# Kernel tuning notes

Measured on AMD Instinct MI355X. Metric: run time of the kernel, lower is better.

Reference implementation:

```python
import jax, jax.numpy as jnp
import numpy as np

N = 1_000_000          # number of query points
POINT_DIMS = 2         # (x, y) coordinates
NUM_EMB = 6572         # number of video frames
EMB_DIM = 32
HIDDEN = 128


def setup_inputs() -> dict:
    key = jax.random.key(0)
    ks = jax.random.split(key, 10)
    x = jax.random.uniform(ks[0], (N, POINT_DIMS), dtype=jnp.float32)
    # fractional frame index in [0, NUM_EMB - 1)
    embeddings = jax.random.uniform(ks[1], (N,), dtype=jnp.float32) * (NUM_EMB - 1)
    em_table = jax.random.normal(ks[2], (NUM_EMB, EMB_DIM), dtype=jnp.float32) * 0.1
    in0 = POINT_DIMS + EMB_DIM
    W0 = jax.random.normal(ks[3], (in0, HIDDEN), dtype=jnp.float32) / np.sqrt(in0)
    b0 = jax.random.normal(ks[4], (HIDDEN,), dtype=jnp.float32) * 0.01
    W1 = jax.random.normal(ks[5], (HIDDEN, HIDDEN), dtype=jnp.float32) / np.sqrt(HIDDEN)
    b1 = jax.random.normal(ks[6], (HIDDEN,), dtype=jnp.float32) * 0.01
    W2 = jax.random.normal(ks[7], (HIDDEN, 1), dtype=jnp.float32) / np.sqrt(HIDDEN)
    b2 = jax.random.normal(ks[8], (1,), dtype=jnp.float32) * 0.01
    return {"x": x, "embeddings": embeddings, "em_table": em_table,
            "W0": W0, "b0": b0, "W1": W1, "b1": b1, "W2": W2, "b2": b2}


def reference(x, embeddings, em_table, W0, b0, W1, b1, W2, b2):
    num_emb = em_table.shape[0]
    em1 = embeddings.astype(jnp.int32)                       # floor (inputs >= 0)
    em2 = jnp.minimum(em1 + 1, num_emb - 1)                  # clamp(em1+1, max=E-1)
    res = (embeddings - em1.astype(jnp.float32))[:, None]    # [N, 1]
    e1 = em_table[em1]                                       # [N, 32] gather
    e2 = em_table[em2]                                       # [N, 32] gather
    em = e1 + (e2 - e1) * res                                # lerp
    h = jnp.concatenate((x, em), axis=1) @ W0 + b0           # [N, 128]
    h = jnp.clip(h, 0.0, 1.0)
    h = jnp.clip(h @ W1 + b1, 0.0, 1.0)
    out = jax.nn.sigmoid(h @ W2 + b2)                        # [N, 1]
    return out
```

## Files before the change

### kernel.cpp

```cpp
#include <hip/hip_runtime.h>
#include <hip/hip_bf16.h>


using bf16x8 = __attribute__((ext_vector_type(8))) short;
using f32x4  = __attribute__((ext_vector_type(4))) float;

#define NPTS    1000000
#define NUMEMB  6572
#define HID     128
#define M_IT    64
#define A0S     72
#define H0S     136
#define TILES   (NPTS / M_IT)
#define NBLOCKS 1024

__device__ __forceinline__ unsigned short bf16r(float f) {
    unsigned u;
    __builtin_memcpy(&u, &f, 4);
    u = (u + 0x7fffu + ((u >> 16) & 1u)) >> 16;
    return (unsigned short)u;
}
__device__ __forceinline__ unsigned pk2(float a, float b) {
    float2 f2; f2.x = a; f2.y = b;
    __hip_bfloat162 h = __float22bfloat162_rn(f2);
    unsigned u;
    __builtin_memcpy(&u, &h, 4);
    return u;
}
__device__ __forceinline__ unsigned pk2c(float a, float b) {
    unsigned r;
    asm("v_cvt_pk_bf16_f32 %0, %1, %2 clamp" : "=v"(r) : "v"(a), "v"(b));
    return r;
}

__global__ __launch_bounds__(256, 4)
void mlp_fused(const float* __restrict__ x,
               const float* __restrict__ emb,
               const float* __restrict__ em_table,
               const float* __restrict__ W0, const float* __restrict__ b0,
               const float* __restrict__ W1, const float* __restrict__ b1,
               const float* __restrict__ W2, const float* __restrict__ b2,
               float* __restrict__ out)
{
    __shared__ __align__(16) unsigned short A0[M_IT * A0S];
    __shared__ __align__(16) unsigned short H0[M_IT * H0S];

    const int tid  = threadIdx.x;
    const int lane = tid & 63;
    const int nq   = tid >> 6;
    const int q    = lane >> 4;
    const int cl   = lane & 15;
    const int p    = tid >> 2;
    const int s    = tid & 3;

    for (int i = tid; i < M_IT * A0S; i += 256) A0[i] = 0;

    const int hcol = nq * 32 + (cl >> 2) * 8 + (cl & 3);
    bf16x8 w0t[2][2];
    for (int hb = 0; hb < 2; ++hb)
        for (int kt = 0; kt < 2; ++kt) {
            const int col = hcol + hb * 4;
            bf16x8 v;
            #pragma unroll
            for (int e = 0; e < 8; ++e) {
                const int k = kt * 32 + q * 8 + e;
                float val = 0.f;
                if (k < 32)       val = W0[(2 + k) * HID + col];
                else if (k == 32) val = W0[0 * HID + col];
                else if (k == 33) val = W0[1 * HID + col];
                v[e] = (short)bf16r(val);
            }
            w0t[hb][kt] = v;
        }

    bf16x8 w1r[2][4];
    for (int hb = 0; hb < 2; ++hb)
        for (int kk = 0; kk < 4; ++kk) {
            const int kt  = (nq + kk) & 3;
            const int col = hcol + hb * 4;
            bf16x8 v;
            #pragma unroll
            for (int e = 0; e < 8; ++e) {
                const int k = kt * 32 + q * 8 + e;
                v[e] = (short)bf16r(W1[k * HID + col]);
            }
            w1r[hb][kk] = v;
        }

    f32x4 b0q[2], b1q[2];
    for (int hb = 0; hb < 2; ++hb)
        for (int r = 0; r < 4; ++r) {
            const int h = nq * 32 + q * 8 + hb * 4 + r;
            b0q[hb][r] = b0[h];
            b1q[hb][r] = b1[h];
        }
    bf16x8 w2f;
    #pragma unroll
    for (int e = 0; e < 8; ++e)
        w2f[e] = (cl == 0) ? (short)bf16r(W2[nq * 32 + q * 8 + e]) : (short)0;
    const float bias2 = b2[0];

    int t = blockIdx.x;
    float  feA;
    float2 xvA = {0.f, 0.f};
    {
        const int gp = t * M_IT + p;
        feA = emb[gp];
        if (s == 0) xvA = *(const float2*)(x + 2 * gp);
    }

    __syncthreads();

    for (; t < TILES; t += gridDim.x) {
        const int base = t * M_IT;

        {
            const int e1 = (int)feA;
            const int e2 = (e1 + 1 < NUMEMB) ? e1 + 1 : NUMEMB - 1;
            const float r = feA - (float)e1;
            const float4* p1 = (const float4*)(em_table + e1 * 32 + s * 8);
            const float4* p2 = (const float4*)(em_table + e2 * 32 + s * 8);
            const float4 a0v = p1[0], a1v = p1[1];
            const float4 c0v = p2[0], c1v = p2[1];
            uint4 d;
            d.x = pk2(a0v.x + (c0v.x - a0v.x) * r, a0v.y + (c0v.y - a0v.y) * r);
            d.y = pk2(a0v.z + (c0v.z - a0v.z) * r, a0v.w + (c0v.w - a0v.w) * r);
            d.z = pk2(a1v.x + (c1v.x - a1v.x) * r, a1v.y + (c1v.y - a1v.y) * r);
            d.w = pk2(a1v.z + (c1v.z - a1v.z) * r, a1v.w + (c1v.w - a1v.w) * r);
            *(uint4*)&A0[p * A0S + s * 8] = d;
            if (s == 0) *(unsigned*)&A0[p * A0S + 32] = pk2(xvA.x, xvA.y);
        }
        __syncthreads();

        f32x4 acc[4][2];
        #pragma unroll
        for (int pb = 0; pb < 4; ++pb) {
            const bf16x8 bf0 = *(const bf16x8*)&A0[(pb * 16 + cl) * A0S + q * 8];
            const bf16x8 bf1 = *(const bf16x8*)&A0[(pb * 16 + cl) * A0S + 32 + q * 8];
            #pragma unroll
            for (int hb = 0; hb < 2; ++hb) {
                f32x4 a = __builtin_amdgcn_mfma_f32_16x16x32_bf16(
                    w0t[hb][0], bf0, b0q[hb], 0, 0, 0);
                acc[pb][hb] = __builtin_amdgcn_mfma_f32_16x16x32_bf16(
                    w0t[hb][1], bf1, a, 0, 0, 0);
            }
        }

        {
            int t1 = t + gridDim.x; if (t1 >= TILES) t1 = t;
            const int gp = t1 * M_IT + p;
            feA = emb[gp];
            if (s == 0) xvA = *(const float2*)(x + 2 * gp);
        }

        #pragma unroll
        for (int pb = 0; pb < 4; ++pb) {
            const f32x4 v0 = acc[pb][0], v1 = acc[pb][1];
            uint4 w;
            w.x = pk2c(v0[0], v0[1]);
            w.y = pk2c(v0[2], v0[3]);
            w.z = pk2c(v1[0], v1[1]);
            w.w = pk2c(v1[2], v1[3]);
            *(uint4*)&H0[(pb * 16 + cl) * H0S + nq * 32 + q * 8] = w;
        }
        __syncthreads();

        #pragma unroll
        for (int kk = 0; kk < 4; ++kk) {
            const int kcol = (((nq + kk) & 3) << 5) + q * 8;
            #pragma unroll
            for (int pb = 0; pb < 4; ++pb) {
                bf16x8 bfrag = *(const bf16x8*)
                    &H0[(pb * 16 + cl) * H0S + kcol];
                #pragma unroll
                for (int hb = 0; hb < 2; ++hb)
                    acc[pb][hb] = __builtin_amdgcn_mfma_f32_16x16x32_bf16(
                        w1r[hb][kk], bfrag,
                        kk == 0 ? b1q[hb] : acc[pb][hb], 0, 0, 0);
            }
        }

        const f32x4 zero = {0.f, 0.f, 0.f, 0.f};
        #pragma unroll
        for (int pb = 0; pb < 4; ++pb) {
            const f32x4 v0 = acc[pb][0], v1 = acc[pb][1];
            uint4 w;
            w.x = pk2c(v0[0], v0[1]);
            w.y = pk2c(v0[2], v0[3]);
            w.z = pk2c(v1[0], v1[1]);
            w.w = pk2c(v1[2], v1[3]);
            bf16x8 hf;
            __builtin_memcpy(&hf, &w, 16);
            const f32x4 z4 = __builtin_amdgcn_mfma_f32_16x16x32_bf16(
                w2f, hf, zero, 0, 0, 0);
            if (q == 0)
                *(float*)((char*)A0 + (pb * 16 + cl) * 144 + 128 + nq * 4) = z4[0];
        }
        __syncthreads();

        if (tid < 64) {
            const float4 pv = *(const float4*)((const char*)A0 + tid * 144 + 128);
            const float zz = bias2 + pv.x + pv.y + pv.z + pv.w;
            out[base + tid] = __builtin_amdgcn_rcpf(1.f + __expf(-zz));
        }
    }
}

extern "C" void kernel_launch(void* const* d_in, const int* in_sizes, int n_in,
                              void* d_out, int out_size, void* d_ws, size_t ws_size,
                              hipStream_t stream) {
    const float* x   = (const float*)d_in[0];
    const float* emb = (const float*)d_in[1];
    const float* emt = (const float*)d_in[2];
    const float* W0  = (const float*)d_in[3];
    const float* b0  = (const float*)d_in[4];
    const float* W1  = (const float*)d_in[5];
    const float* b1  = (const float*)d_in[6];
    const float* W2  = (const float*)d_in[7];
    const float* b2  = (const float*)d_in[8];
    mlp_fused<<<NBLOCKS, 256, 0, stream>>>(x, emb, emt, W0, b0, W1, b1, W2, b2,
                                           (float*)d_out);
}
```

Before: 136.0 us.

## Restructure MLP into single-wave blocks with register-resident hidden layers and gather prefetch

Each block becomes one 64-lane wave that handles 16 points per step and holds all W0/W1 fragments in registers. The first-layer activations pass directly as MFMA B-operands for layer two, so the LDS H0 staging and all block-wide barriers go away. The embedding gather is software-pipelined two chunks ahead and uses a double-buffered A0 tile. In exchange, register pressure rises sharply (w1t alone is 32 bf16x8 vectors), which may limit occupancy or cause spills. Only 1024 single-wave blocks are launched, so latency hiding depends on the prefetch.

```diff
diff --git a/kernel.cpp b/kernel.cpp
--- a/kernel.cpp
+++ b/kernel.cpp
@@ -8,11 +8,11 @@
 #define NPTS    1000000
 #define NUMEMB  6572
 #define HID     128
-#define M_IT    64
 #define A0S     72
-#define H0S     136
-#define TILES   (NPTS / M_IT)
+#define CHUNKS  62500
+#define LASTC   (CHUNKS - 1)
 #define NBLOCKS 1024
+#define STRIDE  1024
 
 __device__ __forceinline__ unsigned short bf16r(float f) {
     unsigned u;
@@ -33,7 +33,7 @@
     return r;
 }
 
-__global__ __launch_bounds__(256, 4)
+__global__ __launch_bounds__(64, 1)
 void mlp_fused(const float* __restrict__ x,
                const float* __restrict__ emb,
                const float* __restrict__ em_table,
@@ -42,24 +42,22 @@
                const float* __restrict__ W2, const float* __restrict__ b2,
                float* __restrict__ out)
 {
-    __shared__ __align__(16) unsigned short A0[M_IT * A0S];
-    __shared__ __align__(16) unsigned short H0[M_IT * H0S];
-
-    const int tid  = threadIdx.x;
-    const int lane = tid & 63;
-    const int nq   = tid >> 6;
-    const int q    = lane >> 4;
-    const int cl   = lane & 15;
-    const int p    = tid >> 2;
-    const int s    = tid & 3;
-
-    for (int i = tid; i < M_IT * A0S; i += 256) A0[i] = 0;
-
-    const int hcol = nq * 32 + (cl >> 2) * 8 + (cl & 3);
-    bf16x8 w0t[2][2];
-    for (int hb = 0; hb < 2; ++hb)
+    __shared__ __align__(16) unsigned short A0[2 * 16 * A0S];
+
+    const int lane = threadIdx.x;
+    const int q  = lane >> 4;
+    const int cl = lane & 15;
+    const int p  = lane >> 2;
+    const int s  = lane & 3;
+
+    for (int i = lane; i < 2 * 16 * A0S; i += 64) A0[i] = 0;
+
+    bf16x8 w0t[8][2];
+    #pragma unroll
+    for (int ob = 0; ob < 8; ++ob) {
+        const int col = (ob >> 1) * 32 + (cl >> 2) * 8 + (ob & 1) * 4 + (cl & 3);
+        #pragma unroll
         for (int kt = 0; kt < 2; ++kt) {
-            const int col = hcol + hb * 4;
             bf16x8 v;
             #pragma unroll
             for (int e = 0; e < 8; ++e) {
@@ -70,120 +68,153 @@
                 else if (k == 33) val = W0[1 * HID + col];
                 v[e] = (short)bf16r(val);
             }
-            w0t[hb][kt] = v;
-        }
-
-    bf16x8 w1r[2][4];
-    for (int hb = 0; hb < 2; ++hb)
-        for (int kk = 0; kk < 4; ++kk) {
-            const int kt  = (nq + kk) & 3;
-            const int col = hcol + hb * 4;
+            w0t[ob][kt] = v;
+        }
+    }
+    bf16x8 w1t[8][4];
+    #pragma unroll
+    for (int ob = 0; ob < 8; ++ob) {
+        const int col = (ob >> 1) * 32 + (cl >> 2) * 8 + (ob & 1) * 4 + (cl & 3);
+        #pragma unroll
+        for (int kt = 0; kt < 4; ++kt) {
             bf16x8 v;
             #pragma unroll
-            for (int e = 0; e < 8; ++e) {
-                const int k = kt * 32 + q * 8 + e;
-                v[e] = (short)bf16r(W1[k * HID + col]);
-            }
-            w1r[hb][kk] = v;
-        }
-
-    f32x4 b0q[2], b1q[2];
-    for (int hb = 0; hb < 2; ++hb)
+            for (int e = 0; e < 8; ++e)
+                v[e] = (short)bf16r(W1[(kt * 32 + q * 8 + e) * HID + col]);
+            w1t[ob][kt] = v;
+        }
+    }
+    f32x4 b0q[8], b1q[8];
+    #pragma unroll
+    for (int ob = 0; ob < 8; ++ob) {
+        #pragma unroll
         for (int r = 0; r < 4; ++r) {
-            const int h = nq * 32 + q * 8 + hb * 4 + r;
-            b0q[hb][r] = b0[h];
-            b1q[hb][r] = b1[h];
-        }
-    bf16x8 w2f;
-    #pragma unroll
-    for (int e = 0; e < 8; ++e)
-        w2f[e] = (cl == 0) ? (short)bf16r(W2[nq * 32 + q * 8 + e]) : (short)0;
+            const int h = (ob >> 1) * 32 + q * 8 + (ob & 1) * 4 + r;
+            b0q[ob][r] = b0[h];
+            b1q[ob][r] = b1[h];
+        }
+    }
+    bf16x8 w2f[4];
+    #pragma unroll
+    for (int kt = 0; kt < 4; ++kt) {
+        #pragma unroll
+        for (int e = 0; e < 8; ++e)
+            w2f[kt][e] = (cl == 0) ? (short)bf16r(W2[kt * 32 + q * 8 + e])
+                                   : (short)0;
+    }
     const float bias2 = b2[0];
 
-    int t = blockIdx.x;
-    float  feA;
-    float2 xvA = {0.f, 0.f};
+    int c = blockIdx.x;
+
     {
-        const int gp = t * M_IT + p;
-        feA = emb[gp];
-        if (s == 0) xvA = *(const float2*)(x + 2 * gp);
-    }
-
-    __syncthreads();
-
-    for (; t < TILES; t += gridDim.x) {
-        const int base = t * M_IT;
+        const int gp = c * 16 + p;
+        const float fe0 = emb[gp];
+        float2 xv0 = {0.f, 0.f};
+        if (s == 0) xv0 = *(const float2*)(x + 2 * gp);
+        const int e1 = (int)fe0;
+        const int e2 = (e1 + 1 < NUMEMB) ? e1 + 1 : NUMEMB - 1;
+        const float r = fe0 - (float)e1;
+        const float4* p1 = (const float4*)(em_table + e1 * 32 + s * 8);
+        const float4* p2 = (const float4*)(em_table + e2 * 32 + s * 8);
+        const float4 a0v = p1[0], a1v = p1[1];
+        const float4 c0v = p2[0], c1v = p2[1];
+        uint4 d;
+        d.x = pk2(a0v.x + (c0v.x - a0v.x) * r, a0v.y + (c0v.y - a0v.y) * r);
+        d.y = pk2(a0v.z + (c0v.z - a0v.z) * r, a0v.w + (c0v.w - a0v.w) * r);
+        d.z = pk2(a1v.x + (c1v.x - a1v.x) * r, a1v.y + (c1v.y - a1v.y) * r);
+        d.w = pk2(a1v.z + (c1v.z - a1v.z) * r, a1v.w + (c1v.w - a1v.w) * r);
+        *(uint4*)&A0[p * A0S + s * 8] = d;
+        if (s == 0) *(unsigned*)&A0[p * A0S + 32] = pk2(xv0.x, xv0.y);
+    }
+
+    int cA = c + STRIDE;     if (cA > LASTC) cA = LASTC;
+    int cB = c + 2 * STRIDE; if (cB > LASTC) cB = LASTC;
+    const float feA = emb[cA * 16 + p];
+    float feB = emb[cB * 16 + p];
+    float2 xvA = {0.f, 0.f}, xvB = {0.f, 0.f};
+    if (s == 0) {
+        xvA = *(const float2*)(x + 2 * (cA * 16 + p));
+        xvB = *(const float2*)(x + 2 * (cB * 16 + p));
+    }
+    float4 g1a, g1b, g2a, g2b;
+    float frA;
+    {
+        const int e1 = (int)feA;
+        const int e2 = (e1 + 1 < NUMEMB) ? e1 + 1 : NUMEMB - 1;
+        frA = feA - (float)e1;
+        const float4* p1 = (const float4*)(em_table + e1 * 32 + s * 8);
+        const float4* p2 = (const float4*)(em_table + e2 * 32 + s * 8);
+        g1a = p1[0]; g1b = p1[1]; g2a = p2[0]; g2b = p2[1];
+    }
+
+    int buf = 0;
+    for (; c < CHUNKS; c += STRIDE) {
+        const int rowR = (buf * 16 + cl) * A0S;
+        const bf16x8 bf0 = *(const bf16x8*)&A0[rowR + q * 8];
+        const bf16x8 bf1 = *(const bf16x8*)&A0[rowR + 32 + q * 8];
 
         {
-            const int e1 = (int)feA;
+            const int rowW = ((buf ^ 1) * 16 + p) * A0S;
+            uint4 d;
+            d.x = pk2(g1a.x + (g2a.x - g1a.x) * frA, g1a.y + (g2a.y - g1a.y) * frA);
+            d.y = pk2(g1a.z + (g2a.z - g1a.z) * frA, g1a.w + (g2a.w - g1a.w) * frA);
+            d.z = pk2(g1b.x + (g2b.x - g1b.x) * frA, g1b.y + (g2b.y - g1b.y) * frA);
+            d.w = pk2(g1b.z + (g2b.z - g1b.z) * frA, g1b.w + (g2b.w - g1b.w) * frA);
+            *(uint4*)&A0[rowW + s * 8] = d;
+            if (s == 0) *(unsigned*)&A0[rowW + 32] = pk2(xvA.x, xvA.y);
+        }
+
+        {
+            const int e1 = (int)feB;
             const int e2 = (e1 + 1 < NUMEMB) ? e1 + 1 : NUMEMB - 1;
-            const float r = feA - (float)e1;
+            frA = feB - (float)e1;
             const float4* p1 = (const float4*)(em_table + e1 * 32 + s * 8);
             const float4* p2 = (const float4*)(em_table + e2 * 32 + s * 8);
-            const float4 a0v = p1[0], a1v = p1[1];
-            const float4 c0v = p2[0], c1v = p2[1];
-            uint4 d;
-            d.x = pk2(a0v.x + (c0v.x - a0v.x) * r, a0v.y + (c0v.y - a0v.y) * r);
-            d.y = pk2(a0v.z + (c0v.z - a0v.z) * r, a0v.w + (c0v.w - a0v.w) * r);
-            d.z = pk2(a1v.x + (c1v.x - a1v.x) * r, a1v.y + (c1v.y - a1v.y) * r);
-            d.w = pk2(a1v.z + (c1v.z - a1v.z) * r, a1v.w + (c1v.w - a1v.w) * r);
-            *(uint4*)&A0[p * A0S + s * 8] = d;
-            if (s == 0) *(unsigned*)&A0[p * A0S + 32] = pk2(xvA.x, xvA.y);
-        }
-        __syncthreads();
-
-        f32x4 acc[4][2];
-        #pragma unroll
-        for (int pb = 0; pb < 4; ++pb) {
-            const bf16x8 bf0 = *(const bf16x8*)&A0[(pb * 16 + cl) * A0S + q * 8];
-            const bf16x8 bf1 = *(const bf16x8*)&A0[(pb * 16 + cl) * A0S + 32 + q * 8];
-            #pragma unroll
-            for (int hb = 0; hb < 2; ++hb) {
-                f32x4 a = __builtin_amdgcn_mfma_f32_16x16x32_bf16(
-                    w0t[hb][0], bf0, b0q[hb], 0, 0, 0);
-                acc[pb][hb] = __builtin_amdgcn_mfma_f32_16x16x32_bf16(
-                    w0t[hb][1], bf1, a, 0, 0, 0);
-            }
-        }
-
-        {
-            int t1 = t + gridDim.x; if (t1 >= TILES) t1 = t;
-            const int gp = t1 * M_IT + p;
-            feA = emb[gp];
-            if (s == 0) xvA = *(const float2*)(x + 2 * gp);
-        }
-
-        #pragma unroll
-        for (int pb = 0; pb < 4; ++pb) {
-            const f32x4 v0 = acc[pb][0], v1 = acc[pb][1];
+            g1a = p1[0]; g1b = p1[1]; g2a = p2[0]; g2b = p2[1];
+            xvA = xvB;
+            int cC = c + 3 * STRIDE; if (cC > LASTC) cC = LASTC;
+            feB = emb[cC * 16 + p];
+            if (s == 0) xvB = *(const float2*)(x + 2 * (cC * 16 + p));
+        }
+
+        f32x4 acc[8];
+        #pragma unroll
+        for (int ob = 0; ob < 8; ++ob)
+            acc[ob] = __builtin_amdgcn_mfma_f32_16x16x32_bf16(
+                w0t[ob][0], bf0, b0q[ob], 0, 0, 0);
+        #pragma unroll
+        for (int ob = 0; ob < 8; ++ob)
+            acc[ob] = __builtin_amdgcn_mfma_f32_16x16x32_bf16(
+                w0t[ob][1], bf1, acc[ob], 0, 0, 0);
+
+        bf16x8 h1f[4];
+        #pragma unroll
+        for (int kt = 0; kt < 4; ++kt) {
+            const f32x4 v0 = acc[2 * kt], v1 = acc[2 * kt + 1];
             uint4 w;
             w.x = pk2c(v0[0], v0[1]);
             w.y = pk2c(v0[2], v0[3]);
             w.z = pk2c(v1[0], v1[1]);
             w.w = pk2c(v1[2], v1[3]);
-            *(uint4*)&H0[(pb * 16 + cl) * H0S + nq * 32 + q * 8] = w;
-        }
-        __syncthreads();
-
-        #pragma unroll
-        for (int kk = 0; kk < 4; ++kk) {
-            const int kcol = (((nq + kk) & 3) << 5) + q * 8;
+            __builtin_memcpy(&h1f[kt], &w, 16);
+        }
+
+        #pragma unroll
+        for (int ob = 0; ob < 8; ++ob)
+            acc[ob] = __builtin_amdgcn_mfma_f32_16x16x32_bf16(
+                w1t[ob][0], h1f[0], b1q[ob], 0, 0, 0);
+        #pragma unroll
+        for (int kt = 1; kt < 4; ++kt)
             #pragma unroll
-            for (int pb = 0; pb < 4; ++pb) {
-                bf16x8 bfrag = *(const bf16x8*)
-                    &H0[(pb * 16 + cl) * H0S + kcol];
-                #pragma unroll
-                for (int hb = 0; hb < 2; ++hb)
-                    acc[pb][hb] = __builtin_amdgcn_mfma_f32_16x16x32_bf16(
-                        w1r[hb][kk], bfrag,
-                        kk == 0 ? b1q[hb] : acc[pb][hb], 0, 0, 0);
-            }
-        }
+            for (int ob = 0; ob < 8; ++ob)
+                acc[ob] = __builtin_amdgcn_mfma_f32_16x16x32_bf16(
+                    w1t[ob][kt], h1f[kt], acc[ob], 0, 0, 0);
 
         const f32x4 zero = {0.f, 0.f, 0.f, 0.f};
-        #pragma unroll
-        for (int pb = 0; pb < 4; ++pb) {
-            const f32x4 v0 = acc[pb][0], v1 = acc[pb][1];
+        f32x4 za = zero, zb = zero;
+        #pragma unroll
+        for (int kt = 0; kt < 4; ++kt) {
+            const f32x4 v0 = acc[2 * kt], v1 = acc[2 * kt + 1];
             uint4 w;
             w.x = pk2c(v0[0], v0[1]);
             w.y = pk2c(v0[2], v0[3]);
@@ -191,18 +222,16 @@
             w.w = pk2c(v1[2], v1[3]);
             bf16x8 hf;
             __builtin_memcpy(&hf, &w, 16);
-            const f32x4 z4 = __builtin_amdgcn_mfma_f32_16x16x32_bf16(
-                w2f, hf, zero, 0, 0, 0);
-            if (q == 0)
-                *(float*)((char*)A0 + (pb * 16 + cl) * 144 + 128 + nq * 4) = z4[0];
-        }
-        __syncthreads();
-
-        if (tid < 64) {
-            const float4 pv = *(const float4*)((const char*)A0 + tid * 144 + 128);
-            const float zz = bias2 + pv.x + pv.y + pv.z + pv.w;
-            out[base + tid] = __builtin_amdgcn_rcpf(1.f + __expf(-zz));
-        }
+            if (kt < 2)
+                za = __builtin_amdgcn_mfma_f32_16x16x32_bf16(w2f[kt], hf, za, 0, 0, 0);
+            else
+                zb = __builtin_amdgcn_mfma_f32_16x16x32_bf16(w2f[kt], hf, zb, 0, 0, 0);
+        }
+        const float z = za[0] + zb[0] + bias2;
+        const float sig = __builtin_amdgcn_rcpf(1.f + __expf(-z));
+        if (q == 0) out[c * 16 + cl] = sig;
+
+        buf ^= 1;
     }
 }
 
@@ -218,6 +247,6 @@
     const float* b1  = (const float*)d_in[6];
     const float* W2  = (const float*)d_in[7];
     const float* b2  = (const float*)d_in[8];
-    mlp_fused<<<NBLOCKS, 256, 0, stream>>>(x, emb, emt, W0, b0, W1, b1, W2, b2,
-                                           (float*)d_out);
-}
+    mlp_fused<<<NBLOCKS, 64, 0, stream>>>(x, emb, emt, W0, b0, W1, b1, W2, b2,
+                                          (float*)d_out);
+}
```

Result: slower. 143.8 us (+5.7%).
